# Optimization experiments

Hardware: AMD Instinct MI355X
Metric: run time of the kernel (lower is better)

## Reference

```python
import jax, jax.numpy as jnp
import numpy as np

P = 8  # patch size hardcoded in FSAS/DFFN
EPS = 1e-5


def conv1x1(x, w):
    # x: [B,C,H,W], w: [Cout,Cin]
    return jnp.einsum('bchw,oc->bohw', x, w)


def dwconv3(x, w):
    # depthwise 3x3, w: [C,1,3,3]
    return jax.lax.conv_general_dilated(
        x, w, window_strides=(1, 1), padding='SAME',
        dimension_numbers=('NCHW', 'OIHW', 'NCHW'),
        feature_group_count=x.shape[1])


def layernorm_c(x, w, b):
    # WithBias LayerNorm over channel dim (torch: b c h w -> b (h w) c, LN over c)
    mu = jnp.mean(x, axis=1, keepdims=True)
    var = jnp.var(x, axis=1, keepdims=True)
    return (x - mu) / jnp.sqrt(var + EPS) * w[None, :, None, None] + b[None, :, None, None]


def to_patches(x):
    # [B,C,H,W] -> [B,C,H/P,W/P,P,P]
    B, C, H, W = x.shape
    return x.reshape(B, C, H // P, P, W // P, P).transpose(0, 1, 2, 4, 3, 5)


def from_patches(xp):
    B, C, h, w, p1, p2 = xp.shape
    return xp.transpose(0, 1, 2, 4, 3, 5).reshape(B, C, h * p1, w * p2)


def fsas(x, w_hidden, dw, norm_w, norm_b, w_out):
    hidden = conv1x1(x, w_hidden)          # [B,6d,H,W]
    qkv = dwconv3(hidden, dw)
    q, k, v = jnp.split(qkv, 3, axis=1)    # each [B,2d,H,W]
    qf = jnp.fft.rfft2(to_patches(q))
    kf = jnp.fft.rfft2(to_patches(k))
    out = jnp.fft.irfft2(qf * kf, s=(P, P))
    out = layernorm_c(from_patches(out), norm_w, norm_b)
    return conv1x1(v * out, w_out)


def dffn(x, w_in, fft_w, dw, w_out):
    x = conv1x1(x, w_in)                   # [B,2h,H,W]
    xf = jnp.fft.rfft2(to_patches(x))
    # fft_w: [2h,1,1,P,P//2+1] broadcasts against [B,2h,h,w,P,P//2+1]
    x = from_patches(jnp.fft.irfft2(xf * fft_w, s=(P, P)))
    x1, x2 = jnp.split(dwconv3(x, dw), 2, axis=1)
    return conv1x1(jax.nn.gelu(x1, approximate=False) * x2, w_out)


def setup_inputs() -> dict:
    key = jax.random.key(0)
    ks = jax.random.split(key, 10)
    d = 48
    h = int(d * 3)  # ffn_expansion_factor=3 -> hidden_features=144
    B, H, W = 2, 256, 256

    def n(k, shape, s=0.05):
        return jax.random.normal(k, shape, jnp.float32) * s

    return {
        'x': jax.random.normal(ks[0], (B, d, H, W), jnp.float32),
        'norm1_w': jnp.ones((d,), jnp.float32),
        'norm1_b': jnp.zeros((d,), jnp.float32),
        'attn_w_hidden': n(ks[1], (6 * d, d)),
        'attn_dw': n(ks[2], (6 * d, 1, 3, 3), 0.2),
        'attn_norm_w': jnp.ones((2 * d,), jnp.float32),
        'attn_norm_b': jnp.zeros((2 * d,), jnp.float32),
        'attn_w_out': n(ks[3], (d, 2 * d)),
        'norm2_w': jnp.ones((d,), jnp.float32),
        'norm2_b': jnp.zeros((d,), jnp.float32),
        'ffn_w_in': n(ks[4], (2 * h, d)),
        'ffn_fft': 1.0 + n(ks[5], (2 * h, 1, 1, P, P // 2 + 1), 0.1),
        'ffn_dw': n(ks[6], (2 * h, 1, 3, 3), 0.2),
        'ffn_w_out': n(ks[7], (d, h)),
    }


def reference(x, norm1_w, norm1_b, attn_w_hidden, attn_dw, attn_norm_w,
              attn_norm_b, attn_w_out, norm2_w, norm2_b, ffn_w_in, ffn_fft,
              ffn_dw, ffn_w_out):
    x = x + fsas(layernorm_c(x, norm1_w, norm1_b),
                 attn_w_hidden, attn_dw, attn_norm_w, attn_norm_b, attn_w_out)
    x = x + dffn(layernorm_c(x, norm2_w, norm2_b),
                 ffn_w_in, ffn_fft, ffn_dw, ffn_w_out)
    return x
```

## Files before the change

kernel.cpp:

```cpp
#include <hip/hip_runtime.h>
#include <hip/hip_bf16.h>
#include <cstddef>


constexpr int HWC = 65536;

typedef short short8 __attribute__((ext_vector_type(8)));
typedef __bf16 bf16x8 __attribute__((ext_vector_type(8)));
typedef float f32x4 __attribute__((ext_vector_type(4)));

__device__ inline unsigned short f2bf(float f) {
  __hip_bfloat16 h = __float2bfloat16(f);
  return *reinterpret_cast<unsigned short*>(&h);
}
__device__ inline float bf2f(unsigned short u) {
  __hip_bfloat16 h;
  *reinterpret_cast<unsigned short*>(&h) = u;
  return __bfloat162float(h);
}

union V8 { uint4 v; unsigned short us[8]; };

__device__ inline void load8f(const unsigned short* p, float* f) {
  V8 u; u.v = *reinterpret_cast<const uint4*>(p);
#pragma unroll
  for (int j = 0; j < 8; j++) f[j] = bf2f(u.us[j]);
}
__device__ inline void store8bf(unsigned short* p, const float* f) {
  V8 u;
#pragma unroll
  for (int j = 0; j < 8; j++) u.us[j] = f2bf(f[j]);
  *reinterpret_cast<uint4*>(p) = u.v;
}

__global__ __launch_bounds__(64) void k_prep_w(
    const float* __restrict__ awh, const float* __restrict__ awo,
    const float* __restrict__ fwi, const float* __restrict__ fwo,
    unsigned short* __restrict__ wp) {
  int row = blockIdx.x, t = threadIdx.x;
  const float* src; int K, KP; unsigned short* dst;
  if (row < 288)      { src = awh + row * 48;        K = 48;  KP = 64;
                        dst = wp + row * 64; }
  else if (row < 336) { int r = row - 288; src = awo + r * 96; K = 96; KP = 96;
                        dst = wp + 18432 + r * 96; }
  else if (row < 624) { int r = row - 336; src = fwi + r * 48; K = 48; KP = 64;
                        dst = wp + 23040 + r * 64; }
  else                { int r = row - 624; src = fwo + r * 144; K = 144; KP = 160;
                        dst = wp + 41472 + r * 160; }
  for (int k = t; k < KP; k += 64) dst[k] = f2bf(k < K ? src[k] : 0.f);
}

template <int M, int K, int KP, int XF, int EPI>
__global__ __launch_bounds__(256) void k_gemm(
    const unsigned short* __restrict__ wb, const void* __restrict__ s1,
    const unsigned short* __restrict__ s2, const float* __restrict__ lnw,
    const float* __restrict__ lnb, const void* __restrict__ res,
    void* __restrict__ out) {
  constexpr int STRIDE = KP + 8;
  constexpr int KS = KP / 32;
  constexpr int NT = (M + 63) / 64;
  __shared__ __align__(16) short Xs[64 * STRIDE];
  __shared__ __align__(16) short Vs[(XF == 2) ? 64 * STRIDE : 4];
  __shared__ float redS[4][64], redS2[4][64], mus[64], invs[64];

  int tid = threadIdx.x;
  unsigned bid = blockIdx.x;
  int b = (int)(bid >> 10);
  int hw0 = (int)(bid & 1023) * 64;

  if (XF == 1) {
    const float* xp = (const float*)s1 + (size_t)b * 48 * HWC + hw0;
    for (int idx = tid; idx < 48 * 16; idx += 256) {
      int c = idx >> 4, colg = (idx & 15) * 4;
      float4 f = *reinterpret_cast<const float4*>(xp + (size_t)c * HWC + colg);
      Xs[(colg + 0) * STRIDE + c] = (short)f2bf(f.x);
      Xs[(colg + 1) * STRIDE + c] = (short)f2bf(f.y);
      Xs[(colg + 2) * STRIDE + c] = (short)f2bf(f.z);
      Xs[(colg + 3) * STRIDE + c] = (short)f2bf(f.w);
    }
  } else if (XF == 2) {
    const unsigned short* up =
        (const unsigned short*)s1 + (size_t)b * 96 * HWC + hw0;
    const unsigned short* vp = s2 + ((size_t)(b * 288 + 192)) * HWC + hw0;
    for (int idx = tid; idx < 96 * 16; idx += 256) {
      int c = idx >> 4, colg = (idx & 15) * 4;
      ushort4 uv = *reinterpret_cast<const ushort4*>(up + (size_t)c * HWC + colg);
      Xs[(colg + 0) * STRIDE + c] = (short)uv.x;
      Xs[(colg + 1) * STRIDE + c] = (short)uv.y;
      Xs[(colg + 2) * STRIDE + c] = (short)uv.z;
      Xs[(colg + 3) * STRIDE + c] = (short)uv.w;
      ushort4 vv = *reinterpret_cast<const ushort4*>(vp + (size_t)c * HWC + colg);
      Vs[(colg + 0) * STRIDE + c] = (short)vv.x;
      Vs[(colg + 1) * STRIDE + c] = (short)vv.y;
      Vs[(colg + 2) * STRIDE + c] = (short)vv.z;
      Vs[(colg + 3) * STRIDE + c] = (short)vv.w;
    }
  } else if (XF == 3) {
    const unsigned short* xp =
        (const unsigned short*)s1 + (size_t)b * 48 * HWC + hw0;
    for (int idx = tid; idx < 48 * 16; idx += 256) {
      int c = idx >> 4, colg = (idx & 15) * 4;
      ushort4 uv = *reinterpret_cast<const ushort4*>(xp + (size_t)c * HWC + colg);
      Xs[(colg + 0) * STRIDE + c] = (short)uv.x;
      Xs[(colg + 1) * STRIDE + c] = (short)uv.y;
      Xs[(colg + 2) * STRIDE + c] = (short)uv.z;
      Xs[(colg + 3) * STRIDE + c] = (short)uv.w;
    }
  } else {
    const unsigned short* p1 =
        (const unsigned short*)s1 + (size_t)b * 96 * HWC + hw0;
    const unsigned short* p2 = s2 + (size_t)b * 48 * HWC + hw0;
    for (int idx = tid; idx < K * 16; idx += 256) {
      int c = idx >> 4, colg = (idx & 15) * 4;
      const unsigned short* p =
          (c < 96) ? (p1 + (size_t)c * HWC + colg)
                   : (p2 + (size_t)(c - 96) * HWC + colg);
      ushort4 uv = *reinterpret_cast<const ushort4*>(p);
      Xs[(colg + 0) * STRIDE + c] = (short)uv.x;
      Xs[(colg + 1) * STRIDE + c] = (short)uv.y;
      Xs[(colg + 2) * STRIDE + c] = (short)uv.z;
      Xs[(colg + 3) * STRIDE + c] = (short)uv.w;
    }
  }

  if constexpr (KP > K) {
    constexpr int PAD = KP - K;
    for (int idx = tid; idx < 64 * PAD; idx += 256) {
      int col = idx / PAD, c = K + (idx % PAD);
      Xs[col * STRIDE + c] = 0;
    }
  }

  if (XF != 0) {
    constexpr int KC = (XF == 2) ? 96 : 48;
    __syncthreads();
    {
      int col = tid & 63, q = tid >> 6;
      float s = 0.f, s2 = 0.f;
      for (int c = q * (KC / 4); c < (q + 1) * (KC / 4); c++) {
        float v = bf2f((unsigned short)Xs[col * STRIDE + c]);
        s += v; s2 += v * v;
      }
      redS[q][col] = s; redS2[q][col] = s2;
    }
    __syncthreads();
    if (tid < 64) {
      float ss = redS[0][tid] + redS[1][tid] + redS[2][tid] + redS[3][tid];
      float ss2 = redS2[0][tid] + redS2[1][tid] + redS2[2][tid] + redS2[3][tid];
      float mu = ss * (1.f / KC);
      float var = ss2 * (1.f / KC) - mu * mu;
      mus[tid] = mu; invs[tid] = rsqrtf(var + 1e-5f);
    }
    __syncthreads();
    for (int idx = tid; idx < KC * 64; idx += 256) {
      int c = idx >> 6, col = idx & 63;
      float v = bf2f((unsigned short)Xs[col * STRIDE + c]);
      v = (v - mus[col]) * invs[col] * lnw[c] + lnb[c];
      if (XF == 2) v *= bf2f((unsigned short)Vs[col * STRIDE + c]);
      Xs[col * STRIDE + c] = (short)f2bf(v);
    }
  }
  __syncthreads();

  int lane = tid & 63, wvi = tid >> 6;
  int quad = lane >> 4, mc = lane & 15;
  int kbase = quad * 8;

  short8 bfr[4][KS];
#pragma unroll
  for (int ns = 0; ns < 4; ns++)
#pragma unroll
    for (int ks = 0; ks < KS; ks++)
      bfr[ns][ks] = *reinterpret_cast<const short8*>(
          Xs + (ns * 16 + mc) * STRIDE + ks * 32 + kbase);

#pragma unroll
  for (int t = 0; t < NT; t++) {
    int mb = (wvi + 4 * t) * 16;
    if (mb >= M) continue;
    short8 afr[KS];
#pragma unroll
    for (int ks = 0; ks < KS; ks++)
      afr[ks] = *reinterpret_cast<const short8*>(
          wb + (size_t)(mb + mc) * KP + ks * 32 + kbase);
#pragma unroll
    for (int ns = 0; ns < 4; ns++) {
      f32x4 acc = {0.f, 0.f, 0.f, 0.f};
#pragma unroll
      for (int ks = 0; ks < KS; ks++)
        acc = __builtin_amdgcn_mfma_f32_16x16x32_bf16(
            __builtin_bit_cast(bf16x8, afr[ks]),
            __builtin_bit_cast(bf16x8, bfr[ns][ks]), acc, 0, 0, 0);
      int hw = hw0 + ns * 16 + mc;
#pragma unroll
      for (int r = 0; r < 4; r++) {
        int m = mb + quad * 4 + r;
        if (EPI == 0) {
          ((unsigned short*)out)[((size_t)(b * M + m)) * HWC + hw] =
              f2bf(acc[r]);
        } else if (EPI == 1) {
          float rv = ((const float*)res)[((size_t)(b * 48 + m)) * HWC + hw];
          ((unsigned short*)out)[((size_t)(b * 48 + m)) * HWC + hw] =
              f2bf(rv + acc[r]);
        } else {
          float rv = bf2f(
              ((const unsigned short*)res)[((size_t)(b * 48 + m)) * HWC + hw]);
          ((float*)out)[((size_t)(b * 48 + m)) * HWC + hw] = rv + acc[r];
        }
      }
    }
  }
}

__global__ __launch_bounds__(256) void k_dwconv3(
    const unsigned short* __restrict__ in, const float* __restrict__ dw,
    unsigned short* __restrict__ out) {
  int tid = threadIdx.x;
  unsigned bid = blockIdx.x;
  int y0 = (int)(bid & 31) * 8;
  unsigned t = bid >> 5;
  int c = (int)(t % 288u);
  int b = (int)(t / 288u);
  const unsigned short* ip = in + ((size_t)(b * 288 + c)) * HWC;
  float wv[9];
#pragma unroll
  for (int k = 0; k < 9; k++) wv[k] = dw[c * 9 + k];
  int r = tid >> 5, seg = tid & 31, lane = tid & 63;
  int y = y0 + r;
  float f[3][8];
#pragma unroll
  for (int dy = 0; dy < 3; dy++) {
    int yy = y + dy - 1;
    if (yy >= 0 && yy < 256) {
      load8f(ip + yy * 256 + seg * 8, f[dy]);
    } else {
#pragma unroll
      for (int j = 0; j < 8; j++) f[dy][j] = 0.f;
    }
  }
  float o[8];
#pragma unroll
  for (int dy = 0; dy < 3; dy++) {
    float lv = __shfl(f[dy][7], lane - 1, 64);
    float rv = __shfl(f[dy][0], lane + 1, 64);
    if (seg == 0) lv = 0.f;
    if (seg == 31) rv = 0.f;
#pragma unroll
    for (int j = 0; j < 8; j++) {
      float xl = (j == 0) ? lv : f[dy][j - 1];
      float xr = (j == 7) ? rv : f[dy][j + 1];
      float v = xl * wv[dy * 3] + f[dy][j] * wv[dy * 3 + 1] + xr * wv[dy * 3 + 2];
      o[j] = (dy == 0) ? v : o[j] + v;
    }
  }
  store8bf(out + ((size_t)(b * 288 + c)) * HWC + y * 256 + seg * 8, o);
}

__global__ __launch_bounds__(256) void k_fsas_patchconv(
    const unsigned short* __restrict__ qkv, unsigned short* __restrict__ out) {
  __shared__ float qs[8][296];
  __shared__ float kt[8][296];
  int tid = threadIdx.x;
  unsigned bid = blockIdx.x;
  int py = (int)(bid & 31);
  int c = (int)((bid >> 5) % 96u);
  int b = (int)((bid >> 5) / 96u);
  const unsigned short* qp = qkv + ((size_t)(b * 288 + c)) * HWC + py * 2048;
  const unsigned short* kp =
      qkv + ((size_t)(b * 288 + 96 + c)) * HWC + py * 2048;
  {
    int rr = tid >> 5, seg = tid & 31;
    float fq[8], fk[8];
    load8f(qp + rr * 256 + seg * 8, fq);
    load8f(kp + rr * 256 + seg * 8, fk);
#pragma unroll
    for (int j = 0; j < 8; j++) {
      qs[rr][seg * 9 + j] = fq[j];
      kt[rr][seg * 9 + j] = fk[j];
    }
  }
  __syncthreads();
  int p = tid >> 3, a = tid & 7;
  float acc[8];
#pragma unroll
  for (int j = 0; j < 8; j++) acc[j] = 0.f;
#pragma unroll
  for (int i = 0; i < 8; i++) {
    float q8[8], k8[8];
#pragma unroll
    for (int j = 0; j < 8; j++) q8[j] = qs[i][p * 9 + j];
    int ar = (a - i) & 7;
#pragma unroll
    for (int j = 0; j < 8; j++) k8[j] = kt[ar][p * 9 + j];
#pragma unroll
    for (int j = 0; j < 8; j++)
#pragma unroll
      for (int bb = 0; bb < 8; bb++) acc[bb] += q8[j] * k8[(bb - j) & 7];
  }
  store8bf(out + ((size_t)(b * 96 + c)) * HWC + (py * 8 + a) * 256 + p * 8,
           acc);
}

__device__ const float c_cos8[8] = {
    1.f, 0.70710678118654752f, 0.f, -0.70710678118654752f,
    -1.f, -0.70710678118654752f, 0.f, 0.70710678118654752f};

__global__ __launch_bounds__(64) void k_make_cmat(
    const float* __restrict__ fftw, unsigned short* __restrict__ cmat) {
  __shared__ float sf[64];
  int c = blockIdx.x;
  int a = threadIdx.x >> 3, b2 = threadIdx.x & 7;
  const float* W = fftw + c * 40;
  float acc = 0.f;
  for (int u = 0; u < 8; u++) {
    for (int v = 0; v < 8; v++) {
      float wv;
      if (v <= 4) {
        if (v == 0 || v == 4)
          wv = 0.5f * (W[u * 5 + v] + W[((8 - u) & 7) * 5 + v]);
        else
          wv = W[u * 5 + v];
      } else {
        wv = W[((8 - u) & 7) * 5 + (8 - v)];
      }
      acc += wv * c_cos8[(u * a + v * b2) & 7];
    }
  }
  sf[threadIdx.x] = acc * (1.f / 64.f);
  __syncthreads();
  unsigned short* cp = cmat + (size_t)c * 4096 + threadIdx.x * 64;
  for (int k8 = 0; k8 < 64; k8 += 8) {
    float v[8];
    int ka = k8 >> 3;
    int ia = ((a - ka) & 7) * 8;
#pragma unroll
    for (int j = 0; j < 8; j++) v[j] = sf[ia + ((b2 - j) & 7)];
    store8bf(cp + k8, v);
  }
}

__global__ __launch_bounds__(256) void k_patchconv_mfma(
    unsigned short* y, const unsigned short* __restrict__ cmat) {
  __shared__ __align__(16) short Bs[32 * 72];
  __shared__ __align__(16) short As[64 * 72];
  int tid = threadIdx.x;
  unsigned bid = blockIdx.x;
  int py = (int)(bid & 31);
  int c = (int)((bid >> 5) % 288u);
  int b = (int)((bid >> 5) / 288u);
  unsigned short* yp = y + ((size_t)(b * 288 + c)) * HWC + py * 2048;
  {
    int rr = tid >> 5, seg = tid & 31;
    *reinterpret_cast<uint4*>(Bs + seg * 72 + rr * 8) =
        *reinterpret_cast<const uint4*>(yp + rr * 256 + seg * 8);
  }
  {
    const unsigned short* cp = cmat + (size_t)c * 4096;
    int m = tid >> 2, kq = (tid & 3) * 16;
    *reinterpret_cast<uint4*>(As + m * 72 + kq) =
        *reinterpret_cast<const uint4*>(cp + m * 64 + kq);
    *reinterpret_cast<uint4*>(As + m * 72 + kq + 8) =
        *reinterpret_cast<const uint4*>(cp + m * 64 + kq + 8);
  }
  __syncthreads();
  int lane = tid & 63, wvi = tid >> 6;
  int quad = lane >> 4, mc = lane & 15;
  int kbase = quad * 8;
  short8 afr[2];
#pragma unroll
  for (int ks = 0; ks < 2; ks++)
    afr[ks] = *reinterpret_cast<const short8*>(
        As + (wvi * 16 + mc) * 72 + ks * 32 + kbase);
#pragma unroll
  for (int nt = 0; nt < 2; nt++) {
    short8 bfr[2];
#pragma unroll
    for (int ks = 0; ks < 2; ks++)
      bfr[ks] = *reinterpret_cast<const short8*>(
          Bs + (nt * 16 + mc) * 72 + ks * 32 + kbase);
    f32x4 acc = {0.f, 0.f, 0.f, 0.f};
#pragma unroll
    for (int ks = 0; ks < 2; ks++)
      acc = __builtin_amdgcn_mfma_f32_16x16x32_bf16(
          __builtin_bit_cast(bf16x8, afr[ks]),
          __builtin_bit_cast(bf16x8, bfr[ks]), acc, 0, 0, 0);
    int p = nt * 16 + mc;
    int m0 = wvi * 16 + quad * 4;
    int a = m0 >> 3, b8 = m0 & 7;
    ushort4 pk;
    pk.x = f2bf(acc[0]); pk.y = f2bf(acc[1]);
    pk.z = f2bf(acc[2]); pk.w = f2bf(acc[3]);
    *reinterpret_cast<ushort4*>(yp + a * 256 + p * 8 + b8) = pk;
  }
}

__global__ __launch_bounds__(256) void k_ffn_gate(
    const unsigned short* __restrict__ z, const float* __restrict__ dwf,
    unsigned short* __restrict__ g1, unsigned short* __restrict__ g2) {
  int tid = threadIdx.x;
  unsigned bid = blockIdx.x;
  int y0 = (int)(bid & 31) * 8;
  unsigned t = bid >> 5;
  int c = (int)(t % 144u);
  int b = (int)(t / 144u);
  const unsigned short* zp1 = z + ((size_t)(b * 288 + c)) * HWC;
  const unsigned short* zp2 = z + ((size_t)(b * 288 + 144 + c)) * HWC;
  float w1[9], w2[9];
#pragma unroll
  for (int k = 0; k < 9; k++) {
    w1[k] = dwf[c * 9 + k];
    w2[k] = dwf[(144 + c) * 9 + k];
  }
  int r = tid >> 5, seg = tid & 31, lane = tid & 63;
  int y = y0 + r;
  float f1[3][8], f2[3][8];
#pragma unroll
  for (int dy = 0; dy < 3; dy++) {
    int yy = y + dy - 1;
    if (yy >= 0 && yy < 256) {
      load8f(zp1 + yy * 256 + seg * 8, f1[dy]);
      load8f(zp2 + yy * 256 + seg * 8, f2[dy]);
    } else {
#pragma unroll
      for (int j = 0; j < 8; j++) { f1[dy][j] = 0.f; f2[dy][j] = 0.f; }
    }
  }
  float d1[8], d2[8];
#pragma unroll
  for (int j = 0; j < 8; j++) { d1[j] = 0.f; d2[j] = 0.f; }
#pragma unroll
  for (int dy = 0; dy < 3; dy++) {
    float lv1 = __shfl(f1[dy][7], lane - 1, 64);
    float rv1 = __shfl(f1[dy][0], lane + 1, 64);
    float lv2 = __shfl(f2[dy][7], lane - 1, 64);
    float rv2 = __shfl(f2[dy][0], lane + 1, 64);
    if (seg == 0) { lv1 = 0.f; lv2 = 0.f; }
    if (seg == 31) { rv1 = 0.f; rv2 = 0.f; }
#pragma unroll
    for (int j = 0; j < 8; j++) {
      float xl1 = (j == 0) ? lv1 : f1[dy][j - 1];
      float xr1 = (j == 7) ? rv1 : f1[dy][j + 1];
      float xl2 = (j == 0) ? lv2 : f2[dy][j - 1];
      float xr2 = (j == 7) ? rv2 : f2[dy][j + 1];
      d1[j] += xl1 * w1[dy * 3] + f1[dy][j] * w1[dy * 3 + 1] + xr1 * w1[dy * 3 + 2];
      d2[j] += xl2 * w2[dy * 3] + f2[dy][j] * w2[dy * 3 + 1] + xr2 * w2[dy * 3 + 2];
    }
  }
  float o[8];
#pragma unroll
  for (int j = 0; j < 8; j++)
    o[j] = 0.5f * d1[j] * (1.f + erff(d1[j] * 0.70710678118654752f)) * d2[j];
  unsigned short* gp = (c < 96)
      ? g1 + ((size_t)(b * 96 + c)) * HWC
      : g2 + ((size_t)(b * 48 + (c - 96))) * HWC;
  store8bf(gp + y * 256 + seg * 8, o);
}

extern "C" void kernel_launch(void* const* d_in, const int* in_sizes, int n_in,
                              void* d_out, int out_size, void* d_ws,
                              size_t ws_size, hipStream_t stream) {
  (void)in_sizes; (void)n_in; (void)out_size; (void)ws_size;
  const float* x   = (const float*)d_in[0];
  const float* n1w = (const float*)d_in[1];
  const float* n1b = (const float*)d_in[2];
  const float* awh = (const float*)d_in[3];
  const float* adw = (const float*)d_in[4];
  const float* anw = (const float*)d_in[5];
  const float* anb = (const float*)d_in[6];
  const float* awo = (const float*)d_in[7];
  const float* n2w = (const float*)d_in[8];
  const float* n2b = (const float*)d_in[9];
  const float* fwi = (const float*)d_in[10];
  const float* fff = (const float*)d_in[11];
  const float* fdw = (const float*)d_in[12];
  const float* fwo = (const float*)d_in[13];

  unsigned short* QKV  = (unsigned short*)d_ws;
  unsigned short* HID  = (unsigned short*)((char*)d_ws + 75497472);
  unsigned short* U    = (unsigned short*)((char*)d_ws + 150994944);
  unsigned short* X1   = (unsigned short*)((char*)d_ws + 176160768);
  unsigned short* G2   = (unsigned short*)((char*)d_ws + 188743680);
  unsigned short* CMAT = G2;
  unsigned short* WP   = (unsigned short*)((char*)d_ws + 201326592);
  unsigned short* WA = WP;
  unsigned short* WO = WP + 18432;
  unsigned short* WI = WP + 23040;
  unsigned short* WF = WP + 41472;

  k_prep_w<<<672, 64, 0, stream>>>(awh, awo, fwi, fwo, WP);
  k_make_cmat<<<288, 64, 0, stream>>>(fff, CMAT);
  k_gemm<288, 48, 64, 1, 0><<<2048, 256, 0, stream>>>(WA, x, nullptr, n1w,
                                                      n1b, nullptr, HID);
  k_dwconv3<<<2 * 288 * 32, 256, 0, stream>>>(HID, adw, QKV);
  k_fsas_patchconv<<<2 * 96 * 32, 256, 0, stream>>>(QKV, U);
  k_gemm<48, 96, 96, 2, 1><<<2048, 256, 0, stream>>>(WO, U, QKV, anw, anb, x,
                                                     X1);
  k_gemm<288, 48, 64, 3, 0><<<2048, 256, 0, stream>>>(WI, X1, nullptr, n2w,
                                                      n2b, nullptr, QKV);
  k_patchconv_mfma<<<2 * 288 * 32, 256, 0, stream>>>(QKV, CMAT);
  k_ffn_gate<<<2 * 144 * 32, 256, 0, stream>>>(QKV, fdw, U, G2);
  k_gemm<48, 144, 160, 0, 2><<<2048, 256, 0, stream>>>(WF, U, G2, nullptr,
                                                       nullptr, X1,
                                                       (float*)d_out);
}
```

Baseline: 298.0 us.

## Fuse q/k depthwise conv into FSAS patch conv and stage GEMM epilogue via LDS

The depthwise 3x3 conv for the q and k channels is now computed inside the FSAS patch-convolution kernel straight from the hidden tensor. This removes the write and re-read of two thirds of the QKV intermediate. The standalone dwconv now only handles the v channels. Separately, the GEMM epilogue writes its accumulators through shared memory so each thread can do 16-byte vectorized global stores and residual loads instead of scattered 2-byte ones. The cost is two extra block barriers per output tile and an extra bf16 rounding before the residual add.

```diff
diff --git a/kernel.cpp b/kernel.cpp
--- a/kernel.cpp
+++ b/kernel.cpp
@@ -19,7 +19,7 @@
   return __bfloat162float(h);
 }
 
-union V8 { uint4 v; unsigned short us[8]; };
+union V8 { uint4 v; unsigned short us[8]; short s[8]; };
 
 __device__ inline void load8f(const unsigned short* p, float* f) {
   V8 u; u.v = *reinterpret_cast<const uint4*>(p);
@@ -174,53 +174,93 @@
       bfr[ns][ks] = *reinterpret_cast<const short8*>(
           Xs + (ns * 16 + mc) * STRIDE + ks * 32 + kbase);
 
+  short* Es = Xs;
 #pragma unroll
   for (int t = 0; t < NT; t++) {
     int mb = (wvi + 4 * t) * 16;
-    if (mb >= M) continue;
-    short8 afr[KS];
-#pragma unroll
-    for (int ks = 0; ks < KS; ks++)
-      afr[ks] = *reinterpret_cast<const short8*>(
-          wb + (size_t)(mb + mc) * KP + ks * 32 + kbase);
-#pragma unroll
-    for (int ns = 0; ns < 4; ns++) {
-      f32x4 acc = {0.f, 0.f, 0.f, 0.f};
+    f32x4 accs[4];
+    if (mb < M) {
+      short8 afr[KS];
 #pragma unroll
       for (int ks = 0; ks < KS; ks++)
-        acc = __builtin_amdgcn_mfma_f32_16x16x32_bf16(
-            __builtin_bit_cast(bf16x8, afr[ks]),
-            __builtin_bit_cast(bf16x8, bfr[ns][ks]), acc, 0, 0, 0);
-      int hw = hw0 + ns * 16 + mc;
-#pragma unroll
-      for (int r = 0; r < 4; r++) {
-        int m = mb + quad * 4 + r;
+        afr[ks] = *reinterpret_cast<const short8*>(
+            wb + (size_t)(mb + mc) * KP + ks * 32 + kbase);
+#pragma unroll
+      for (int ns = 0; ns < 4; ns++) {
+        f32x4 acc = {0.f, 0.f, 0.f, 0.f};
+#pragma unroll
+        for (int ks = 0; ks < KS; ks++)
+          acc = __builtin_amdgcn_mfma_f32_16x16x32_bf16(
+              __builtin_bit_cast(bf16x8, afr[ks]),
+              __builtin_bit_cast(bf16x8, bfr[ns][ks]), acc, 0, 0, 0);
+        accs[ns] = acc;
+      }
+    }
+    __syncthreads();
+    if (mb < M) {
+      int chl = wvi * 16 + quad * 4;
+#pragma unroll
+      for (int ns = 0; ns < 4; ns++)
+#pragma unroll
+        for (int r = 0; r < 4; r++)
+          Es[(chl + r) * 72 + ns * 16 + mc] = (short)f2bf(accs[ns][r]);
+    }
+    __syncthreads();
+#pragma unroll
+    for (int i = 0; i < 2; i++) {
+      int chl = (tid >> 3) + 32 * i;
+      int px0 = (tid & 7) * 8;
+      int m = 64 * t + chl;
+      if (m < M) {
+        V8 ev;
+        ev.v = *reinterpret_cast<const uint4*>(Es + chl * 72 + px0);
+        size_t off = ((size_t)(b * ((EPI == 0) ? M : 48) + m)) * HWC + hw0 + px0;
         if (EPI == 0) {
-          ((unsigned short*)out)[((size_t)(b * M + m)) * HWC + hw] =
-              f2bf(acc[r]);
+          *reinterpret_cast<uint4*>((unsigned short*)out + off) = ev.v;
         } else if (EPI == 1) {
-          float rv = ((const float*)res)[((size_t)(b * 48 + m)) * HWC + hw];
-          ((unsigned short*)out)[((size_t)(b * 48 + m)) * HWC + hw] =
-              f2bf(rv + acc[r]);
+          const float* rp = (const float*)res + off;
+          float4 ra = *reinterpret_cast<const float4*>(rp);
+          float4 rb = *reinterpret_cast<const float4*>(rp + 4);
+          V8 pk;
+          pk.us[0] = f2bf(ra.x + bf2f(ev.us[0]));
+          pk.us[1] = f2bf(ra.y + bf2f(ev.us[1]));
+          pk.us[2] = f2bf(ra.z + bf2f(ev.us[2]));
+          pk.us[3] = f2bf(ra.w + bf2f(ev.us[3]));
+          pk.us[4] = f2bf(rb.x + bf2f(ev.us[4]));
+          pk.us[5] = f2bf(rb.y + bf2f(ev.us[5]));
+          pk.us[6] = f2bf(rb.z + bf2f(ev.us[6]));
+          pk.us[7] = f2bf(rb.w + bf2f(ev.us[7]));
+          *reinterpret_cast<uint4*>((unsigned short*)out + off) = pk.v;
         } else {
-          float rv = bf2f(
-              ((const unsigned short*)res)[((size_t)(b * 48 + m)) * HWC + hw]);
-          ((float*)out)[((size_t)(b * 48 + m)) * HWC + hw] = rv + acc[r];
+          V8 rv;
+          rv.v = *reinterpret_cast<const uint4*>((const unsigned short*)res + off);
+          float* op = (float*)out + off;
+          float4 oa, ob;
+          oa.x = bf2f(rv.us[0]) + bf2f(ev.us[0]);
+          oa.y = bf2f(rv.us[1]) + bf2f(ev.us[1]);
+          oa.z = bf2f(rv.us[2]) + bf2f(ev.us[2]);
+          oa.w = bf2f(rv.us[3]) + bf2f(ev.us[3]);
+          ob.x = bf2f(rv.us[4]) + bf2f(ev.us[4]);
+          ob.y = bf2f(rv.us[5]) + bf2f(ev.us[5]);
+          ob.z = bf2f(rv.us[6]) + bf2f(ev.us[6]);
+          ob.w = bf2f(rv.us[7]) + bf2f(ev.us[7]);
+          *reinterpret_cast<float4*>(op) = oa;
+          *reinterpret_cast<float4*>(op + 4) = ob;
         }
       }
     }
   }
 }
 
-__global__ __launch_bounds__(256) void k_dwconv3(
+__global__ __launch_bounds__(256) void k_dwconv3v(
     const unsigned short* __restrict__ in, const float* __restrict__ dw,
     unsigned short* __restrict__ out) {
   int tid = threadIdx.x;
   unsigned bid = blockIdx.x;
   int y0 = (int)(bid & 31) * 8;
   unsigned t = bid >> 5;
-  int c = (int)(t % 288u);
-  int b = (int)(t / 288u);
+  int c = 192 + (int)(t % 96u);
+  int b = (int)(t / 96u);
   const unsigned short* ip = in + ((size_t)(b * 288 + c)) * HWC;
   float wv[9];
 #pragma unroll
@@ -256,8 +296,9 @@
   store8bf(out + ((size_t)(b * 288 + c)) * HWC + y * 256 + seg * 8, o);
 }
 
-__global__ __launch_bounds__(256) void k_fsas_patchconv(
-    const unsigned short* __restrict__ qkv, unsigned short* __restrict__ out) {
+__global__ __launch_bounds__(256) void k_fsas_fused(
+    const unsigned short* __restrict__ hid, const float* __restrict__ dw,
+    unsigned short* __restrict__ out) {
   __shared__ float qs[8][296];
   __shared__ float kt[8][296];
   int tid = threadIdx.x;
@@ -265,19 +306,53 @@
   int py = (int)(bid & 31);
   int c = (int)((bid >> 5) % 96u);
   int b = (int)((bid >> 5) / 96u);
-  const unsigned short* qp = qkv + ((size_t)(b * 288 + c)) * HWC + py * 2048;
-  const unsigned short* kp =
-      qkv + ((size_t)(b * 288 + 96 + c)) * HWC + py * 2048;
-  {
-    int rr = tid >> 5, seg = tid & 31;
-    float fq[8], fk[8];
-    load8f(qp + rr * 256 + seg * 8, fq);
-    load8f(kp + rr * 256 + seg * 8, fk);
+  const unsigned short* qp = hid + ((size_t)(b * 288 + c)) * HWC;
+  const unsigned short* kp = hid + ((size_t)(b * 288 + 96 + c)) * HWC;
+  float w1[9], w2[9];
+#pragma unroll
+  for (int k = 0; k < 9; k++) {
+    w1[k] = dw[c * 9 + k];
+    w2[k] = dw[(96 + c) * 9 + k];
+  }
+  int r = tid >> 5, seg = tid & 31, lane = tid & 63;
+  int y = py * 8 + r;
+  float f1[3][8], f2[3][8];
+#pragma unroll
+  for (int dy = 0; dy < 3; dy++) {
+    int yy = y + dy - 1;
+    if (yy >= 0 && yy < 256) {
+      load8f(qp + yy * 256 + seg * 8, f1[dy]);
+      load8f(kp + yy * 256 + seg * 8, f2[dy]);
+    } else {
+#pragma unroll
+      for (int j = 0; j < 8; j++) { f1[dy][j] = 0.f; f2[dy][j] = 0.f; }
+    }
+  }
+  float d1[8], d2[8];
+#pragma unroll
+  for (int j = 0; j < 8; j++) { d1[j] = 0.f; d2[j] = 0.f; }
+#pragma unroll
+  for (int dy = 0; dy < 3; dy++) {
+    float lv1 = __shfl(f1[dy][7], lane - 1, 64);
+    float rv1 = __shfl(f1[dy][0], lane + 1, 64);
+    float lv2 = __shfl(f2[dy][7], lane - 1, 64);
+    float rv2 = __shfl(f2[dy][0], lane + 1, 64);
+    if (seg == 0) { lv1 = 0.f; lv2 = 0.f; }
+    if (seg == 31) { rv1 = 0.f; rv2 = 0.f; }
 #pragma unroll
     for (int j = 0; j < 8; j++) {
-      qs[rr][seg * 9 + j] = fq[j];
-      kt[rr][seg * 9 + j] = fk[j];
-    }
+      float xl1 = (j == 0) ? lv1 : f1[dy][j - 1];
+      float xr1 = (j == 7) ? rv1 : f1[dy][j + 1];
+      float xl2 = (j == 0) ? lv2 : f2[dy][j - 1];
+      float xr2 = (j == 7) ? rv2 : f2[dy][j + 1];
+      d1[j] += xl1 * w1[dy * 3] + f1[dy][j] * w1[dy * 3 + 1] + xr1 * w1[dy * 3 + 2];
+      d2[j] += xl2 * w2[dy * 3] + f2[dy][j] * w2[dy * 3 + 1] + xr2 * w2[dy * 3 + 2];
+    }
+  }
+#pragma unroll
+  for (int j = 0; j < 8; j++) {
+    qs[r][seg * 9 + j] = d1[j];
+    kt[r][seg * 9 + j] = d2[j];
   }
   __syncthreads();
   int p = tid >> 3, a = tid & 7;
@@ -491,8 +566,8 @@
   k_make_cmat<<<288, 64, 0, stream>>>(fff, CMAT);
   k_gemm<288, 48, 64, 1, 0><<<2048, 256, 0, stream>>>(WA, x, nullptr, n1w,
                                                       n1b, nullptr, HID);
-  k_dwconv3<<<2 * 288 * 32, 256, 0, stream>>>(HID, adw, QKV);
-  k_fsas_patchconv<<<2 * 96 * 32, 256, 0, stream>>>(QKV, U);
+  k_dwconv3v<<<2 * 96 * 32, 256, 0, stream>>>(HID, adw, QKV);
+  k_fsas_fused<<<2 * 96 * 32, 256, 0, stream>>>(HID, adw, U);
   k_gemm<48, 96, 96, 2, 1><<<2048, 256, 0, stream>>>(WO, U, QKV, anw, anb, x,
                                                      X1);
   k_gemm<288, 48, 64, 3, 0><<<2048, 256, 0, stream>>>(WI, X1, nullptr, n2w,
```

Measured after the change: 293.1 us. About the same (-1.7%).
